# Performance work log

Hardware: AMD Instinct MI355X
Metric: run time of the kernel (lower is better)

Reference implementation:

```python
import jax, jax.numpy as jnp
import numpy as np

NEG = -1e30  # acts as log(0) without producing NaN gradients


def _ctc_losses(log_probs, targets, input_lengths, target_lengths, blank=0):
    """CTC forward (alpha) recurrence. log_probs: [T,B,C] (log-softmaxed),
    targets: [B,S] int, lengths: [B]. Returns per-sample NLL [B]."""
    T, B, C = log_probs.shape
    S = targets.shape[1]
    L = 2 * S + 1  # expanded label length (blanks interleaved)

    l_idx = jnp.arange(L)
    tgt_idx = jnp.minimum(l_idx // 2, S - 1)  # clip for l=2S (blank anyway)
    is_blank_pos = (l_idx % 2 == 0)
    # ext[b,l]: blank at even l, targets[b, l//2] at odd l
    ext = jnp.where(is_blank_pos[None, :], blank, targets[:, tgt_idx])  # [B,L]

    # gather emission log-probs for expanded labels: [T,B,L]
    logp_ext = jnp.take_along_axis(
        log_probs, jnp.broadcast_to(ext[None], (T, B, L)), axis=2)

    # skip (s-2 -> s) transition allowed iff l>=2, ext[l]!=blank, ext[l]!=ext[l-2]
    ext_m2 = jnp.concatenate([jnp.full((B, 2), -1, ext.dtype), ext[:, :-2]], axis=1)
    skip_ok = (l_idx[None, :] >= 2) & (~is_blank_pos[None, :]) & (ext != ext_m2)  # [B,L]

    L_b = 2 * target_lengths + 1  # [B]
    valid = l_idx[None, :] < L_b[:, None]  # [B,L]

    # t = 0 init: alpha[0]=logp(ext0), alpha[1]=logp(ext1)
    alpha0 = jnp.full((B, L), NEG, log_probs.dtype)
    alpha0 = alpha0.at[:, 0].set(logp_ext[0, :, 0])
    alpha0 = alpha0.at[:, 1].set(logp_ext[0, :, 1])
    alpha0 = jnp.where(valid, alpha0, NEG)

    def step(alpha, xs):
        logp_t, t = xs  # logp_t: [B,L]
        shift1 = jnp.concatenate(
            [jnp.full((B, 1), NEG, alpha.dtype), alpha[:, :-1]], axis=1)
        shift2 = jnp.concatenate(
            [jnp.full((B, 2), NEG, alpha.dtype), alpha[:, :-2]], axis=1)
        shift2 = jnp.where(skip_ok, shift2, NEG)
        m = jnp.maximum(alpha, jnp.maximum(shift1, shift2))
        lse = m + jnp.log(jnp.exp(alpha - m) + jnp.exp(shift1 - m)
                          + jnp.exp(shift2 - m))
        new = lse + logp_t
        active = (t < input_lengths)[:, None]  # freeze alpha once past T_b
        alpha = jnp.where(valid, jnp.where(active, new, alpha), NEG)
        return alpha, None

    alpha_T, _ = jax.lax.scan(step, alpha0, (logp_ext[1:], jnp.arange(1, T)))

    # loss_b = -logsumexp(alpha[L_b-1], alpha[L_b-2]) at frozen t = T_b-1
    last = jnp.take_along_axis(alpha_T, (L_b - 1)[:, None], axis=1)[:, 0]
    prev = jnp.take_along_axis(alpha_T, (L_b - 2)[:, None], axis=1)[:, 0]
    m = jnp.maximum(last, prev)
    final = m + jnp.log(jnp.exp(last - m) + jnp.exp(prev - m))
    return -final  # [B]


def setup_inputs() -> dict:
    key = jax.random.key(0)
    k1, k2, k3 = jax.random.split(key, 3)
    T, B, C, S = 1024, 32, 1024, 128
    log_probs = jax.nn.log_softmax(
        jax.random.normal(k1, (T, B, C), dtype=jnp.float32), axis=-1)
    targets = jax.random.randint(k2, (B, S), 1, C)  # avoid blank=0 in labels
    input_lengths = jnp.full((B,), T, dtype=jnp.int32)
    target_lengths = jax.random.randint(k3, (B,), 64, S + 1)
    return {"log_probs": log_probs, "targets": targets,
            "input_lengths": input_lengths, "target_lengths": target_lengths}


def reference(log_probs, targets, input_lengths, target_lengths):
    losses = _ctc_losses(log_probs, targets, input_lengths, target_lengths, blank=0)
    # reduction='mean': (loss / target_lengths).mean()
    return (losses / target_lengths.astype(losses.dtype)).mean()
```

## Files before the change

### kernel.cpp

```cpp
#include <hip/hip_runtime.h>


#define L2E 1.44269504088896340736f
#define LN2 0.69314718055994530942f

#if defined(__has_builtin)
#if __has_builtin(__builtin_amdgcn_exp2f) && __has_builtin(__builtin_amdgcn_logf)
#define EXP2F(x) __builtin_amdgcn_exp2f(x)
#define LOG2F(x) __builtin_amdgcn_logf(x)
#else
#define EXP2F(x) __builtin_exp2f(x)
#define LOG2F(x) __builtin_log2f(x)
#endif
#else
#define EXP2F(x) __builtin_exp2f(x)
#define LOG2F(x) __builtin_log2f(x)
#endif

__device__ __forceinline__ int wave_imax64(int x) {
#define DPPI(ctrl) { int _t = __builtin_amdgcn_update_dpp(0, x, (ctrl), 0xf, 0xf, true); \
                     x = (x > _t) ? x : _t; }
    DPPI(0x111)
    DPPI(0x112)
    DPPI(0x114)
    DPPI(0x118)
    DPPI(0x142)
    DPPI(0x143)
#undef DPPI
    return __builtin_amdgcn_readlane(x, 63);
}

__global__ __launch_bounds__(256)
void ctc_gather(const float* __restrict__ lp, const int* __restrict__ targets,
                float4* __restrict__ lab4, float4* __restrict__ blk4,
                float* __restrict__ out, int B, int C, int S, int NT4)
{
    __shared__ float rows[4][1028];
    int t4  = blockIdx.x;
    int b   = blockIdx.y;
    int tid = threadIdx.x;
    if (t4 == 0 && b == 0 && tid == 0) out[0] = 0.0f;

    size_t strideT = (size_t)B * C;
    size_t base = (size_t)(4 * t4) * strideT + (size_t)b * C;
    #pragma unroll
    for (int r = 0; r < 4; ++r) {
        float4 v = *reinterpret_cast<const float4*>(lp + base + (size_t)r * strideT + 4 * tid);
        *reinterpret_cast<float4*>(&rows[r][4 * tid]) = v;
    }
    __syncthreads();

    if (tid < S) {
        int tgt = targets[b * S + tid];
        float4 e;
        e.x = EXP2F(rows[0][tgt] * L2E);
        e.y = EXP2F(rows[1][tgt] * L2E);
        e.z = EXP2F(rows[2][tgt] * L2E);
        e.w = EXP2F(rows[3][tgt] * L2E);
        lab4[((size_t)b * NT4 + t4) * S + tid] = e;
    } else if (tid == S) {
        float4 eb;
        eb.x = EXP2F(rows[0][0] * L2E);
        eb.y = EXP2F(rows[1][0] * L2E);
        eb.z = EXP2F(rows[2][0] * L2E);
        eb.w = EXP2F(rows[3][0] * L2E);
        blk4[(size_t)b * NT4 + t4] = eb;
    }
}

__global__ __launch_bounds__(128)
void ctc_fb(const float4* __restrict__ lab4, const float4* __restrict__ blk4,
            const int* __restrict__ targets, const int* __restrict__ tgt_len,
            float* __restrict__ out, int B, int S, int NT4)
{
    int b    = blockIdx.x;
    int tid  = threadIdx.x;
    int wid  = tid >> 6;
    int lane = tid & 63;
    int tl   = tgt_len[b];

    __shared__ double sA[4][64], sB[4][64];
    __shared__ double sAbx, sBxx;
    __shared__ int sDa, sDb;

    int p0 = 2 * lane, p1 = 2 * lane + 1;
    int t_p0 = targets[b * S + p0];
    int t_p1 = targets[b * S + p1];
    double sk0 = 0.0;
    if (lane > 0) sk0 = (t_p0 != targets[b * S + p0 - 1]) ? 1.0 : 0.0;
    double sk1 = (t_p1 != t_p0) ? 1.0 : 0.0;
    bool need_bx = (2 * tl >= 256);

    const float4* Lg = lab4 + (size_t)b * NT4 * S;
    const float4* Bg = blk4 + (size_t)b * NT4;
    const int NH = NT4 >> 1;

    double b0 = 0.0, c0 = 0.0, b1 = 0.0, c1 = 0.0, xx = 0.0;
    int D = 0;

    float4 ae0, ae1, aeb, be0, be1, beb, ce0, ce1, ceb, de0, de1, deb;

#define LOADG(g, E0, E1, EB) { const float4* _Lp = Lg + (size_t)(g) * S; \
    E0 = _Lp[p0]; E1 = _Lp[p1]; EB = Bg[(g)]; }

#define RENORM() { \
    double _lm = fmax(fmax(b0, b1), fmax(fmax(c0, c1), xx)); \
    int _e = (__double2hiint(_lm) >> 20) & 0x7ff; \
    int _d = 1463 - wave_imax64(_e); \
    b0 = ldexp(b0, _d); b1 = ldexp(b1, _d); c0 = ldexp(c0, _d); \
    c1 = ldexp(c1, _d); xx = ldexp(xx, _d); D += _d; }

    if (wid == 0) {
#define A_STEP(E0f, E1f, EBf) { \
    int _lo = __builtin_amdgcn_update_dpp(0, __double2loint(c1), 0x138, 0xf, 0xf, true); \
    int _hi = __builtin_amdgcn_update_dpp(0, __double2hiint(c1), 0x138, 0xf, 0xf, true); \
    double cin = __hiloint2double(_hi, _lo);         \
    double EB = (double)(EBf), E0 = (double)(E0f), E1 = (double)(E1f); \
    double F0 = E0 * sk0, F1 = E1 * sk1; \
    double nb0 = fma(EB, b0, EB * cin); \
    double nc0 = fma(E0, c0, fma(E0, b0, F0 * cin)); \
    double nb1 = fma(EB, b1, EB * c0); \
    double nc1 = fma(E1, c1, fma(E1, b1, F1 * c0)); \
    if (need_bx) xx = fma(EB, xx, EB * c1); \
    b0 = nb0; c0 = nc0; b1 = nb1; c1 = nc1; }
#define AGROUP4(E0, E1, EB) { A_STEP(E0.x, E1.x, EB.x) A_STEP(E0.y, E1.y, EB.y) \
                              A_STEP(E0.z, E1.z, EB.z) A_STEP(E0.w, E1.w, EB.w) }
        LOADG(0, ae0, ae1, aeb) LOADG(1, be0, be1, beb)
        LOADG(2, ce0, ce1, ceb) LOADG(3, de0, de1, deb)
        if (lane == 0) { b0 = (double)aeb.x; c0 = (double)ae0.x; }
        A_STEP(ae0.y, ae1.y, aeb.y)
        A_STEP(ae0.z, ae1.z, aeb.z)
        A_STEP(ae0.w, ae1.w, aeb.w)
        AGROUP4(be0, be1, beb)
        LOADG(4, ae0, ae1, aeb) LOADG(5, be0, be1, beb)
        AGROUP4(ce0, ce1, ceb) AGROUP4(de0, de1, deb)
        RENORM()
        LOADG(6, ce0, ce1, ceb) LOADG(7, de0, de1, deb)
        for (int g = 4; g < NH; g += 4) {
            AGROUP4(ae0, ae1, aeb) AGROUP4(be0, be1, beb)
            if (g + 4 < NH) { LOADG(g + 4, ae0, ae1, aeb) LOADG(g + 5, be0, be1, beb) }
            AGROUP4(ce0, ce1, ceb) AGROUP4(de0, de1, deb)
            RENORM()
            if (g + 6 < NH) { LOADG(g + 6, ce0, ce1, ceb) LOADG(g + 7, de0, de1, deb) }
        }
#undef AGROUP4
#undef A_STEP
        sA[0][lane] = b0; sA[1][lane] = c0; sA[2][lane] = b1; sA[3][lane] = c1;
        if (lane == 63) { sAbx = xx; sDa = D; }
    } else {
#define B_STEP(E0f, E1f, EBf) { \
    double EB = (double)(EBf), E0 = (double)(E0f), E1 = (double)(E1f); \
    double F0 = sk0 * E0, F1 = sk1 * E1; \
    double t0 = EB * b0, t1 = EB * b1, t2 = EB * xx; \
    double _u = fma(F0, c0, t0); \
    int _lo = __builtin_amdgcn_update_dpp(0, __double2loint(_u), 0x130, 0xf, 0xf, true); \
    int _hi = __builtin_amdgcn_update_dpp(0, __double2hiint(_u), 0x130, 0xf, 0xf, true); \
    double uin = __hiloint2double(_hi, _lo);         \
    uin = (lane == 63) ? t2 : uin; \
    double nb0 = fma(E0, c0, t0); \
    double nc0 = fma(E0, c0, fma(F1, c1, t1)); \
    double nb1 = fma(E1, c1, t1); \
    double nc1 = fma(E1, c1, uin); \
    xx = t2; \
    b0 = nb0; c0 = nc0; b1 = nb1; c1 = nc1; }
#define BGROUP4(E0, E1, EB) { B_STEP(E0.w, E1.w, EB.w) B_STEP(E0.z, E1.z, EB.z) \
                              B_STEP(E0.y, E1.y, EB.y) B_STEP(E0.x, E1.x, EB.x) }
#define LOADGB(h, E0, E1, EB) LOADG((NT4 - 1) - (h), E0, E1, EB)
        if (tl < 128) {
            if (lane == (tl >> 1)) { if (tl & 1) b1 = 1.0; else b0 = 1.0; }
        } else {
            xx = 1.0;
        }
        { int q = tl - 1; if (lane == (q >> 1)) { if (q & 1) c1 = 1.0; else c0 = 1.0; } }
        LOADGB(0, ae0, ae1, aeb) LOADGB(1, be0, be1, beb)
        LOADGB(2, ce0, ce1, ceb) LOADGB(3, de0, de1, deb)
        BGROUP4(ae0, ae1, aeb) BGROUP4(be0, be1, beb)
        LOADGB(4, ae0, ae1, aeb) LOADGB(5, be0, be1, beb)
        BGROUP4(ce0, ce1, ceb) BGROUP4(de0, de1, deb)
        RENORM()
        LOADGB(6, ce0, ce1, ceb) LOADGB(7, de0, de1, deb)
        for (int h = 4; h < NH; h += 4) {
            BGROUP4(ae0, ae1, aeb) BGROUP4(be0, be1, beb)
            if (h + 4 < NH) { LOADGB(h + 4, ae0, ae1, aeb) LOADGB(h + 5, be0, be1, beb) }
            BGROUP4(ce0, ce1, ceb) BGROUP4(de0, de1, deb)
            RENORM()
            if (h + 6 < NH) { LOADGB(h + 6, ce0, ce1, ceb) LOADGB(h + 7, de0, de1, deb) }
        }
#undef LOADGB
#undef BGROUP4
#undef B_STEP
        sB[0][lane] = b0; sB[1][lane] = c0; sB[2][lane] = b1; sB[3][lane] = c1;
        if (lane == 0) { sBxx = xx; sDb = D; }
    }
#undef RENORM
#undef LOADG
    __syncthreads();

    if (wid == 0) {
        double dot = sA[0][lane] * sB[0][lane] + sA[1][lane] * sB[1][lane]
                   + sA[2][lane] * sB[2][lane] + sA[3][lane] * sB[3][lane];
        #pragma unroll
        for (int off = 1; off < 64; off <<= 1) dot += __shfl_xor(dot, off);
        if (lane == 0) {
            dot += sAbx * sBxx;
            int ex = ((__double2hiint(dot) >> 20) & 0x7ff) - 1023;
            double mant = ldexp(dot, -ex);
            float lg = LOG2F((float)mant) + (float)ex;
            float loss_b = -LN2 * (lg - (float)(sDa + sDb));
            atomicAdd(out, loss_b / ((float)tl * (float)B));
        }
    }
}

extern "C" void kernel_launch(void* const* d_in, const int* in_sizes, int n_in,
                              void* d_out, int out_size, void* d_ws, size_t ws_size,
                              hipStream_t stream)
{
    const float* lp      = (const float*)d_in[0];
    const int*   targets = (const int*)d_in[1];
    const int*   tgt_len = (const int*)d_in[3];

    int B = in_sizes[2];
    int S = in_sizes[1] / B;
    int T = 1024;
    int C = in_sizes[0] / (T * B);
    int NT4 = T / 4;

    float* ws    = (float*)d_ws;
    float4* lab4 = (float4*)ws;
    size_t labF  = (size_t)B * NT4 * S * 4;
    float4* blk4 = (float4*)(ws + labF);

    dim3 ggrid(NT4, B);
    hipLaunchKernelGGL(ctc_gather, ggrid, dim3(256), 0, stream,
                       lp, targets, lab4, blk4, (float*)d_out, B, C, S, NT4);
    hipLaunchKernelGGL(ctc_fb, dim3(B), dim3(128), 0, stream,
                       lab4, blk4, targets, tgt_len, (float*)d_out, B, S, NT4);
}
```

Measured before the change: 61.11 us.

## Fuse emission gather into forward-backward kernel with producer warps and double-buffered LDS

Merges the gather kernel and the forward-backward kernel into one kernel with 10 waves per batch. Eight producer waves stream log-prob rows from global memory, stage them in LDS, compute exponentiated emissions, and write them into a double-buffered LDS ring. Two consumer waves run the alpha and beta recurrences chunk by chunk, with a block barrier after each chunk. This removes the workspace round trip and one launch, but only 32 blocks remain to pull the whole log-prob tensor from memory, and each chunk adds a block-wide barrier to the serial recurrence. The output is now zeroed with a memset instead of inside the gather kernel.

```diff
diff --git a/kernel.cpp b/kernel.cpp
--- a/kernel.cpp
+++ b/kernel.cpp
@@ -30,78 +30,47 @@
     return __builtin_amdgcn_readlane(x, 63);
 }
 
-__global__ __launch_bounds__(256)
-void ctc_gather(const float* __restrict__ lp, const int* __restrict__ targets,
-                float4* __restrict__ lab4, float4* __restrict__ blk4,
-                float* __restrict__ out, int B, int C, int S, int NT4)
+__global__ __launch_bounds__(640)
+void ctc_fused(const float* __restrict__ lp, const int* __restrict__ targets,
+               const int* __restrict__ tgt_len, float* __restrict__ out,
+               int B, int C, int S)
 {
-    __shared__ float rows[4][1028];
-    int t4  = blockIdx.x;
-    int b   = blockIdx.y;
-    int tid = threadIdx.x;
-    if (t4 == 0 && b == 0 && tid == 0) out[0] = 0.0f;
-
-    size_t strideT = (size_t)B * C;
-    size_t base = (size_t)(4 * t4) * strideT + (size_t)b * C;
-    #pragma unroll
-    for (int r = 0; r < 4; ++r) {
-        float4 v = *reinterpret_cast<const float4*>(lp + base + (size_t)r * strideT + 4 * tid);
-        *reinterpret_cast<float4*>(&rows[r][4 * tid]) = v;
-    }
-    __syncthreads();
-
-    if (tid < S) {
-        int tgt = targets[b * S + tid];
-        float4 e;
-        e.x = EXP2F(rows[0][tgt] * L2E);
-        e.y = EXP2F(rows[1][tgt] * L2E);
-        e.z = EXP2F(rows[2][tgt] * L2E);
-        e.w = EXP2F(rows[3][tgt] * L2E);
-        lab4[((size_t)b * NT4 + t4) * S + tid] = e;
-    } else if (tid == S) {
-        float4 eb;
-        eb.x = EXP2F(rows[0][0] * L2E);
-        eb.y = EXP2F(rows[1][0] * L2E);
-        eb.z = EXP2F(rows[2][0] * L2E);
-        eb.w = EXP2F(rows[3][0] * L2E);
-        blk4[(size_t)b * NT4 + t4] = eb;
-    }
-}
-
-__global__ __launch_bounds__(128)
-void ctc_fb(const float4* __restrict__ lab4, const float4* __restrict__ blk4,
-            const int* __restrict__ targets, const int* __restrict__ tgt_len,
-            float* __restrict__ out, int B, int S, int NT4)
-{
-    int b    = blockIdx.x;
-    int tid  = threadIdx.x;
-    int wid  = tid >> 6;
-    int lane = tid & 63;
-    int tl   = tgt_len[b];
-
+    __shared__ float em[2][2][16][132];
+    __shared__ float stage[8][1024];
     __shared__ double sA[4][64], sB[4][64];
     __shared__ double sAbx, sBxx;
     __shared__ int sDa, sDb;
 
-    int p0 = 2 * lane, p1 = 2 * lane + 1;
-    int t_p0 = targets[b * S + p0];
-    int t_p1 = targets[b * S + p1];
-    double sk0 = 0.0;
-    if (lane > 0) sk0 = (t_p0 != targets[b * S + p0 - 1]) ? 1.0 : 0.0;
-    double sk1 = (t_p1 != t_p0) ? 1.0 : 0.0;
-    bool need_bx = (2 * tl >= 256);
-
-    const float4* Lg = lab4 + (size_t)b * NT4 * S;
-    const float4* Bg = blk4 + (size_t)b * NT4;
-    const int NH = NT4 >> 1;
+    const int b    = blockIdx.x;
+    const int tid  = threadIdx.x;
+    const int wid  = tid >> 6;
+    const int lane = tid & 63;
+    const int tl   = tgt_len[b];
+    const size_t strideT = (size_t)B * C;
+    const float* lpb = lp + (size_t)b * C;
 
     double b0 = 0.0, c0 = 0.0, b1 = 0.0, c1 = 0.0, xx = 0.0;
     int D = 0;
-
-    float4 ae0, ae1, aeb, be0, be1, beb, ce0, ce1, ceb, de0, de1, deb;
-
-#define LOADG(g, E0, E1, EB) { const float4* _Lp = Lg + (size_t)(g) * S; \
-    E0 = _Lp[p0]; E1 = _Lp[p1]; EB = Bg[(g)]; }
+    double sk0 = 0.0, sk1 = 0.0;
+    const bool need_bx = (2 * tl >= 256);
+    if (wid < 2) {
+        int p0 = 2 * lane, p1 = 2 * lane + 1;
+        int t_p0 = targets[b * S + p0];
+        int t_p1 = targets[b * S + p1];
+        if (lane > 0) sk0 = (t_p0 != targets[b * S + p0 - 1]) ? 1.0 : 0.0;
+        sk1 = (t_p1 != t_p0) ? 1.0 : 0.0;
+        if (wid == 1) {
+            if (tl < 128) {
+                if (lane == (tl >> 1)) { if (tl & 1) b1 = 1.0; else b0 = 1.0; }
+            } else xx = 1.0;
+            int q = tl - 1;
+            if (lane == (q >> 1)) { if (q & 1) c1 = 1.0; else c0 = 1.0; }
+        }
+    }
+
+    const int lw = wid - 2;
+    int tg_lo = 0, tg_hi = 0;
+    if (wid >= 2) { tg_lo = targets[b * S + lane]; tg_hi = targets[b * S + 64 + lane]; }
 
 #define RENORM() { \
     double _lm = fmax(fmax(b0, b1), fmax(fmax(c0, c1), xx)); \
@@ -110,7 +79,6 @@
     b0 = ldexp(b0, _d); b1 = ldexp(b1, _d); c0 = ldexp(c0, _d); \
     c1 = ldexp(c1, _d); xx = ldexp(xx, _d); D += _d; }
 
-    if (wid == 0) {
 #define A_STEP(E0f, E1f, EBf) { \
     int _lo = __builtin_amdgcn_update_dpp(0, __double2loint(c1), 0x138, 0xf, 0xf, true); \
     int _hi = __builtin_amdgcn_update_dpp(0, __double2hiint(c1), 0x138, 0xf, 0xf, true); \
@@ -123,31 +91,7 @@
     double nc1 = fma(E1, c1, fma(E1, b1, F1 * c0)); \
     if (need_bx) xx = fma(EB, xx, EB * c1); \
     b0 = nb0; c0 = nc0; b1 = nb1; c1 = nc1; }
-#define AGROUP4(E0, E1, EB) { A_STEP(E0.x, E1.x, EB.x) A_STEP(E0.y, E1.y, EB.y) \
-                              A_STEP(E0.z, E1.z, EB.z) A_STEP(E0.w, E1.w, EB.w) }
-        LOADG(0, ae0, ae1, aeb) LOADG(1, be0, be1, beb)
-        LOADG(2, ce0, ce1, ceb) LOADG(3, de0, de1, deb)
-        if (lane == 0) { b0 = (double)aeb.x; c0 = (double)ae0.x; }
-        A_STEP(ae0.y, ae1.y, aeb.y)
-        A_STEP(ae0.z, ae1.z, aeb.z)
-        A_STEP(ae0.w, ae1.w, aeb.w)
-        AGROUP4(be0, be1, beb)
-        LOADG(4, ae0, ae1, aeb) LOADG(5, be0, be1, beb)
-        AGROUP4(ce0, ce1, ceb) AGROUP4(de0, de1, deb)
-        RENORM()
-        LOADG(6, ce0, ce1, ceb) LOADG(7, de0, de1, deb)
-        for (int g = 4; g < NH; g += 4) {
-            AGROUP4(ae0, ae1, aeb) AGROUP4(be0, be1, beb)
-            if (g + 4 < NH) { LOADG(g + 4, ae0, ae1, aeb) LOADG(g + 5, be0, be1, beb) }
-            AGROUP4(ce0, ce1, ceb) AGROUP4(de0, de1, deb)
-            RENORM()
-            if (g + 6 < NH) { LOADG(g + 6, ce0, ce1, ceb) LOADG(g + 7, de0, de1, deb) }
-        }
-#undef AGROUP4
-#undef A_STEP
-        sA[0][lane] = b0; sA[1][lane] = c0; sA[2][lane] = b1; sA[3][lane] = c1;
-        if (lane == 63) { sAbx = xx; sDa = D; }
-    } else {
+
 #define B_STEP(E0f, E1f, EBf) { \
     double EB = (double)(EBf), E0 = (double)(E0f), E1 = (double)(E1f); \
     double F0 = sk0 * E0, F1 = sk1 * E1; \
@@ -163,39 +107,82 @@
     double nc1 = fma(E1, c1, uin); \
     xx = t2; \
     b0 = nb0; c0 = nc0; b1 = nb1; c1 = nc1; }
-#define BGROUP4(E0, E1, EB) { B_STEP(E0.w, E1.w, EB.w) B_STEP(E0.z, E1.z, EB.z) \
-                              B_STEP(E0.y, E1.y, EB.y) B_STEP(E0.x, E1.x, EB.x) }
-#define LOADGB(h, E0, E1, EB) LOADG((NT4 - 1) - (h), E0, E1, EB)
-        if (tl < 128) {
-            if (lane == (tl >> 1)) { if (tl & 1) b1 = 1.0; else b0 = 1.0; }
+
+    auto produce = [&](int c, int slot) {
+        const float* r0 = lpb + (size_t)(16 * c + 2 * lw)            * strideT;
+        const float* r1 = lpb + (size_t)(16 * c + 2 * lw + 1)        * strideT;
+        const float* r2 = lpb + (size_t)(1023 - (16 * c + 2 * lw))   * strideT;
+        const float* r3 = lpb + (size_t)(1023 - (16 * c + 2 * lw + 1)) * strideT;
+        float4 g0[4], g1[4], g2[4], g3[4];
+        #pragma unroll
+        for (int j = 0; j < 4; ++j) {
+            g0[j] = *(const float4*)(r0 + 4 * lane + 256 * j);
+            g1[j] = *(const float4*)(r1 + 4 * lane + 256 * j);
+            g2[j] = *(const float4*)(r2 + 4 * lane + 256 * j);
+            g3[j] = *(const float4*)(r3 + 4 * lane + 256 * j);
+        }
+#define PROCROW(G, DD, II) { \
+        _Pragma("unroll") \
+        for (int j = 0; j < 4; ++j) \
+            *(float4*)&stage[lw][4 * lane + 256 * j] = G[j]; \
+        float _e0 = EXP2F(stage[lw][tg_lo] * L2E); \
+        float _e1 = EXP2F(stage[lw][tg_hi] * L2E); \
+        em[DD][slot][II][lane]      = _e0; \
+        em[DD][slot][II][64 + lane] = _e1; \
+        if (lane == 0) em[DD][slot][II][128] = EXP2F(stage[lw][0] * L2E); }
+        PROCROW(g0, 0, 2 * lw)
+        PROCROW(g1, 0, 2 * lw + 1)
+        PROCROW(g2, 1, 2 * lw)
+        PROCROW(g3, 1, 2 * lw + 1)
+#undef PROCROW
+    };
+
+    auto fwd_steps = [&](int slot, int ibeg) {
+        const float* emp = &em[0][slot][0][0];
+        #pragma unroll 4
+        for (int i = ibeg; i < 16; ++i) {
+            float2 pr = *(const float2*)(emp + 132 * i + 2 * lane);
+            float  pb = emp[132 * i + 128];
+            A_STEP(pr.x, pr.y, pb)
+        }
+        RENORM()
+    };
+    auto bwd_steps = [&](int slot) {
+        const float* emp = &em[1][slot][0][0];
+        #pragma unroll 4
+        for (int i = 0; i < 16; ++i) {
+            float2 pr = *(const float2*)(emp + 132 * i + 2 * lane);
+            float  pb = emp[132 * i + 128];
+            B_STEP(pr.x, pr.y, pb)
+        }
+        RENORM()
+    };
+
+    if (wid >= 2) produce(0, 0);
+    __syncthreads();
+    for (int c = 0; c < 32; ++c) {
+        if (wid >= 2) {
+            if (c + 1 < 32) produce(c + 1, (c + 1) & 1);
+        } else if (wid == 0) {
+            if (c == 0) {
+                const float* emp = &em[0][0][0][0];
+                if (lane == 0) { b0 = (double)emp[128]; c0 = (double)emp[0]; }
+                fwd_steps(0, 1);
+            } else fwd_steps(c & 1, 0);
         } else {
-            xx = 1.0;
-        }
-        { int q = tl - 1; if (lane == (q >> 1)) { if (q & 1) c1 = 1.0; else c0 = 1.0; } }
-        LOADGB(0, ae0, ae1, aeb) LOADGB(1, be0, be1, beb)
-        LOADGB(2, ce0, ce1, ceb) LOADGB(3, de0, de1, deb)
-        BGROUP4(ae0, ae1, aeb) BGROUP4(be0, be1, beb)
-        LOADGB(4, ae0, ae1, aeb) LOADGB(5, be0, be1, beb)
-        BGROUP4(ce0, ce1, ceb) BGROUP4(de0, de1, deb)
-        RENORM()
-        LOADGB(6, ce0, ce1, ceb) LOADGB(7, de0, de1, deb)
-        for (int h = 4; h < NH; h += 4) {
-            BGROUP4(ae0, ae1, aeb) BGROUP4(be0, be1, beb)
-            if (h + 4 < NH) { LOADGB(h + 4, ae0, ae1, aeb) LOADGB(h + 5, be0, be1, beb) }
-            BGROUP4(ce0, ce1, ceb) BGROUP4(de0, de1, deb)
-            RENORM()
-            if (h + 6 < NH) { LOADGB(h + 6, ce0, ce1, ceb) LOADGB(h + 7, de0, de1, deb) }
-        }
-#undef LOADGB
-#undef BGROUP4
-#undef B_STEP
+            bwd_steps(c & 1);
+        }
+        __syncthreads();
+    }
+
+    if (wid == 0) {
+        sA[0][lane] = b0; sA[1][lane] = c0; sA[2][lane] = b1; sA[3][lane] = c1;
+        if (lane == 63) { sAbx = xx; sDa = D; }
+    } else if (wid == 1) {
         sB[0][lane] = b0; sB[1][lane] = c0; sB[2][lane] = b1; sB[3][lane] = c1;
         if (lane == 0) { sBxx = xx; sDb = D; }
     }
-#undef RENORM
-#undef LOADG
     __syncthreads();
-
     if (wid == 0) {
         double dot = sA[0][lane] * sB[0][lane] + sA[1][lane] * sB[1][lane]
                    + sA[2][lane] * sB[2][lane] + sA[3][lane] * sB[3][lane];
@@ -210,6 +197,9 @@
             atomicAdd(out, loss_b / ((float)tl * (float)B));
         }
     }
+#undef B_STEP
+#undef A_STEP
+#undef RENORM
 }
 
 extern "C" void kernel_launch(void* const* d_in, const int* in_sizes, int n_in,
@@ -224,16 +214,8 @@
     int S = in_sizes[1] / B;
     int T = 1024;
     int C = in_sizes[0] / (T * B);
-    int NT4 = T / 4;
-
-    float* ws    = (float*)d_ws;
-    float4* lab4 = (float4*)ws;
-    size_t labF  = (size_t)B * NT4 * S * 4;
-    float4* blk4 = (float4*)(ws + labF);
-
-    dim3 ggrid(NT4, B);
-    hipLaunchKernelGGL(ctc_gather, ggrid, dim3(256), 0, stream,
-                       lp, targets, lab4, blk4, (float*)d_out, B, C, S, NT4);
-    hipLaunchKernelGGL(ctc_fb, dim3(B), dim3(128), 0, stream,
-                       lab4, blk4, targets, tgt_len, (float*)d_out, B, S, NT4);
+
+    hipMemsetAsync(d_out, 0, sizeof(float), stream);
+    hipLaunchKernelGGL(ctc_fused, dim3(B), dim3(640), 0, stream,
+                       lp, targets, tgt_len, (float*)d_out, B, C, S);
 }
```

Measured after the change: 83.69 us. 1.37x slower.
